# Performance work log

Measured on AMD Instinct MI355X. Metric: run time of the kernel, lower is better.

Reference implementation:

```python
import jax, jax.numpy as jnp
import numpy as np

# Geometry constants (from init_kwargs geo)
VIEWS = 512
NDET = 736
NX = 256
NY = 256
EXTENT = 2
CHANNEL = 1
START_ANGLE = 0.0
END_ANGLE = 2.0 * np.pi
SCALE = (END_ANGLE - START_ANGLE) / (2.0 * VIEWS * EXTENT)
SINO_LEN = VIEWS * NDET            # 376832
IDX_LEN = NX * NY * VIEWS * EXTENT  # 67108864


def setup_inputs() -> dict:
    key = jax.random.key(0)
    k1, k2, k3, k4 = jax.random.split(key, 4)
    x = jax.random.normal(k1, (1, CHANNEL, SINO_LEN), dtype=jnp.float32)
    weight = jax.random.uniform(k2, (IDX_LEN,), dtype=jnp.float32)
    bias = jax.random.normal(k3, (NX * NY,), dtype=jnp.float32)
    indices = jax.random.randint(k4, (IDX_LEN,), 0, SINO_LEN, dtype=jnp.int64)
    return {"x": x, "weight": weight, "bias": bias, "indices": indices}


def reference(x, weight, bias, indices):
    # x: [B, C, views*nDetecU]
    sino = x.reshape(-1, CHANNEL, SINO_LEN)
    # Irregular gather: [B, C, NX*NY*views*extent]
    g = jnp.take(sino, indices, axis=2)
    # Learned per-ray weighting (DotProduct)
    g = g * weight  # broadcast over leading [B, C]
    # Group by voxel, sum over views*extent, scale by angular step
    g = g.reshape(-1, CHANNEL, NX * NY, VIEWS * EXTENT)
    out = jnp.sum(g, axis=3) * jnp.float32(SCALE)
    out = out + bias  # broadcast over [B, C]
    out = out.reshape(-1, CHANNEL, NX, NY)
    out = jnp.flip(out, axis=(2, 3))
    return out
```

## Files before the change

### kernel.cpp

```cpp
#include <hip/hip_runtime.h>
#include <hip/hip_fp16.h>
#include <math.h>
#include <stdint.h>

#define VIEWS 512
#define NDET 736
#define NX 256
#define NY 256
#define EXTENT 2
#define SINO_LEN (VIEWS * NDET)
#define NVOX (NX * NY)
#define PER_VOX (VIEWS * EXTENT)

#define SEGB 65536
#define NPASS 12
#define XWS_BYTES (NPASS * SEGB)
#define XWS_HALVES (XWS_BYTES / 2)

__device__ __constant__ float kScale = (float)(M_PI / 1024.0);

typedef int   v4i __attribute__((ext_vector_type(4)));
typedef float v4f __attribute__((ext_vector_type(4)));

__global__ __launch_bounds__(256) void convert_x_kernel(
    const float* __restrict__ x, ushort* __restrict__ xh)
{
    const int t = blockIdx.x * 256 + threadIdx.x;
    const int e = t * 4;
    ushort4 u;
    if (e < SINO_LEN) {
        const float4 v = *(const float4*)(x + e);
        u.x = __half_as_ushort(__float2half(v.x));
        u.y = __half_as_ushort(__float2half(v.y));
        u.z = __half_as_ushort(__float2half(v.z));
        u.w = __half_as_ushort(__float2half(v.w));
    } else {
        u.x = u.y = u.z = u.w = 0;
    }
    *(ushort4*)(xh + e) = u;
}

__global__ __launch_bounds__(512, 4) void backproj_lds_kernel(
    const ushort* __restrict__ xh,
    const float*  __restrict__ weight,
    const float*  __restrict__ bias,
    const int*    __restrict__ indices,
    float*        __restrict__ out)
{
    extern __shared__ unsigned char xs[];

    const int tid  = threadIdx.x;
    const int lane = tid & 63;
    const int wid  = tid >> 6;
    const int vv   = tid >> 5;
    const int q    = tid & 31;

    const int    vox0  = blockIdx.x * 16;
    const size_t pbase = (size_t)(vox0 + vv) * PER_VOX;

    const v4i* ip = (const v4i*)(indices + pbase);
    const v4f* wp = (const v4f*)(weight + pbase);

    v4i i4[8];
    v4f w4[8];
#pragma unroll
    for (int k = 0; k < 8; ++k) i4[k] = __builtin_nontemporal_load(&ip[q + k * 32]);
#pragma unroll
    for (int k = 0; k < 8; ++k) w4[k] = __builtin_nontemporal_load(&wp[q + k * 32]);
#pragma unroll
    for (int k = 0; k < 8; ++k) {
        i4[k].x <<= 1; i4[k].y <<= 1; i4[k].z <<= 1; i4[k].w <<= 1;
    }

    const unsigned sbase = (unsigned)(wid * 8192 + lane * 16);

    float s = 0.0f;

    for (int p = 0; p < NPASS; ++p) {
        const unsigned loB = (unsigned)p * SEGB;

#pragma unroll
        for (int k = 0; k < 8; ++k) {
            const unsigned off = sbase + (unsigned)(k * 1024);
            __builtin_amdgcn_global_load_lds(
                (const __attribute__((address_space(1))) unsigned int*)
                    ((const unsigned char*)xh + loB + off),
                (__attribute__((address_space(3))) unsigned int*)(xs + off),
                16, 0, 0);
        }
        __syncthreads();

#pragma unroll
        for (int k = 0; k < 8; ++k) {
            {
                const unsigned off = (unsigned)i4[k].x - loB;
                const bool in = off < (unsigned)SEGB;
                const unsigned a = in ? off : 0u;
                const float val = __half2float(*(const __half*)(xs + a));
                s = fmaf(val, in ? w4[k].x : 0.0f, s);
            }
            {
                const unsigned off = (unsigned)i4[k].y - loB;
                const bool in = off < (unsigned)SEGB;
                const unsigned a = in ? off : 0u;
                const float val = __half2float(*(const __half*)(xs + a));
                s = fmaf(val, in ? w4[k].y : 0.0f, s);
            }
            {
                const unsigned off = (unsigned)i4[k].z - loB;
                const bool in = off < (unsigned)SEGB;
                const unsigned a = in ? off : 0u;
                const float val = __half2float(*(const __half*)(xs + a));
                s = fmaf(val, in ? w4[k].z : 0.0f, s);
            }
            {
                const unsigned off = (unsigned)i4[k].w - loB;
                const bool in = off < (unsigned)SEGB;
                const unsigned a = in ? off : 0u;
                const float val = __half2float(*(const __half*)(xs + a));
                s = fmaf(val, in ? w4[k].w : 0.0f, s);
            }
        }
        __syncthreads();
    }

#pragma unroll
    for (int off = 16; off > 0; off >>= 1)
        s += __shfl_xor(s, off, 64);

    if (q == 0) {
        const int v = vox0 + vv;
        out[NVOX - 1 - v] = bias[v] + kScale * s;
    }
}

__global__ __launch_bounds__(256) void backproj_fallback_kernel(
    const float* __restrict__ x,
    const float* __restrict__ weight,
    const float* __restrict__ bias,
    const int*   __restrict__ indices,
    float*       __restrict__ out)
{
    const int wave_in_block = threadIdx.x >> 6;
    const int lane          = threadIdx.x & 63;
    const int v             = blockIdx.x * 4 + wave_in_block;
    const size_t base       = (size_t)v * PER_VOX;

    const v4i* ip = (const v4i*)(indices + base);
    const v4f* wp = (const v4f*)(weight + base);

    v4i i4[4];
#pragma unroll
    for (int k = 0; k < 4; ++k)
        i4[k] = __builtin_nontemporal_load(&ip[lane + k * 64]);

    float g[16];
#pragma unroll
    for (int k = 0; k < 4; ++k) {
        g[4 * k + 0] = x[i4[k].x];
        g[4 * k + 1] = x[i4[k].y];
        g[4 * k + 2] = x[i4[k].z];
        g[4 * k + 3] = x[i4[k].w];
    }

    v4f w4[4];
#pragma unroll
    for (int k = 0; k < 4; ++k)
        w4[k] = __builtin_nontemporal_load(&wp[lane + k * 64]);

    float s = 0.0f;
#pragma unroll
    for (int k = 0; k < 4; ++k) {
        s += g[4 * k + 0] * w4[k].x;
        s += g[4 * k + 1] * w4[k].y;
        s += g[4 * k + 2] * w4[k].z;
        s += g[4 * k + 3] * w4[k].w;
    }

#pragma unroll
    for (int off = 32; off > 0; off >>= 1)
        s += __shfl_down(s, off, 64);

    if (lane == 0)
        out[NVOX - 1 - v] = bias[v] + kScale * s;
}

extern "C" void kernel_launch(void* const* d_in, const int* in_sizes, int n_in,
                              void* d_out, int out_size, void* d_ws, size_t ws_size,
                              hipStream_t stream) {
    const float* x       = (const float*)d_in[0];
    const float* weight  = (const float*)d_in[1];
    const float* bias    = (const float*)d_in[2];
    const int*   indices = (const int*)d_in[3];
    float*       out     = (float*)d_out;

    if (ws_size >= (size_t)XWS_BYTES) {
        ushort* xh = (ushort*)d_ws;
        convert_x_kernel<<<XWS_HALVES / 4 / 256, 256, 0, stream>>>(x, xh);
        backproj_lds_kernel<<<NVOX / 16, 512, SEGB, stream>>>(
            xh, weight, bias, indices, out);
    } else {
        backproj_fallback_kernel<<<NVOX / 4, 256, 0, stream>>>(
            x, weight, bias, indices, out);
    }
}
```

Measured before the change: 613.1 us.

## Use 128KB LDS segments with register-staged prefetch and 1024-thread blocks

Doubles the LDS segment to 128KB so only 6 passes over the fp16 sinogram are needed instead of 12, and grows blocks to 1024 threads covering 32 voxels. The next segment is prefetched into registers while the current one is being gathered from, replacing the direct global-to-LDS loads. Indices are pre-packed with the pass number in high bits so each in-range test is a subtract and compare, and four accumulators are used instead of one. This halves the number of pass barriers and redundant segment loads, but one block fills the 160KB LDS, so occupancy drops to one block per CU and the kernel relies on the dynamic shared memory attribute being accepted.

After: 938.9 us. +53.1%, slower.

```diff
diff --git a/kernel.cpp b/kernel.cpp
--- a/kernel.cpp
+++ b/kernel.cpp
@@ -12,8 +12,8 @@
 #define NVOX (NX * NY)
 #define PER_VOX (VIEWS * EXTENT)
 
-#define SEGB 65536
-#define NPASS 12
+#define SEGB 131072
+#define NPASS 6
 #define XWS_BYTES (NPASS * SEGB)
 #define XWS_HALVES (XWS_BYTES / 2)
 
@@ -40,7 +40,7 @@
     *(ushort4*)(xh + e) = u;
 }
 
-__global__ __launch_bounds__(512, 4) void backproj_lds_kernel(
+__global__ __launch_bounds__(1024, 4) void backproj_lds2_kernel(
     const ushort* __restrict__ xh,
     const float*  __restrict__ weight,
     const float*  __restrict__ bias,
@@ -49,81 +49,100 @@
 {
     extern __shared__ unsigned char xs[];
 
-    const int tid  = threadIdx.x;
-    const int lane = tid & 63;
-    const int wid  = tid >> 6;
-    const int vv   = tid >> 5;
-    const int q    = tid & 31;
-
-    const int    vox0  = blockIdx.x * 16;
+    const int tid = threadIdx.x;
+    const int vv  = tid >> 5;
+    const int q   = tid & 31;
+
+    const int    vox0  = blockIdx.x * 32;
     const size_t pbase = (size_t)(vox0 + vv) * PER_VOX;
 
     const v4i* ip = (const v4i*)(indices + pbase);
     const v4f* wp = (const v4f*)(weight + pbase);
 
-    v4i i4[8];
+    v4i pk[8];
     v4f w4[8];
 #pragma unroll
-    for (int k = 0; k < 8; ++k) i4[k] = __builtin_nontemporal_load(&ip[q + k * 32]);
+    for (int k = 0; k < 8; ++k) pk[k] = __builtin_nontemporal_load(&ip[q + k * 32]);
 #pragma unroll
     for (int k = 0; k < 8; ++k) w4[k] = __builtin_nontemporal_load(&wp[q + k * 32]);
+
 #pragma unroll
     for (int k = 0; k < 8; ++k) {
-        i4[k].x <<= 1; i4[k].y <<= 1; i4[k].z <<= 1; i4[k].w <<= 1;
-    }
-
-    const unsigned sbase = (unsigned)(wid * 8192 + lane * 16);
-
-    float s = 0.0f;
-
+        int b;
+        b = pk[k].x << 1; pk[k].x = ((b >> 17) << 20) | (b & (SEGB - 1));
+        b = pk[k].y << 1; pk[k].y = ((b >> 17) << 20) | (b & (SEGB - 1));
+        b = pk[k].z << 1; pk[k].z = ((b >> 17) << 20) | (b & (SEGB - 1));
+        b = pk[k].w << 1; pk[k].w = ((b >> 17) << 20) | (b & (SEGB - 1));
+    }
+
+    float4 r[8];
+    const unsigned soff = (unsigned)tid * 16;
+
+#define ISSUE(SEG)                                                          \
+    {                                                                       \
+        const unsigned char* gp = (const unsigned char*)xh +                \
+                                  (size_t)(SEG) * SEGB;                     \
+        _Pragma("unroll")                                                   \
+        for (int k = 0; k < 8; ++k)                                         \
+            r[k] = *(const float4*)(gp + (unsigned)(k * 16384) + soff);     \
+    }
+#define COMMIT()                                                            \
+    {                                                                       \
+        _Pragma("unroll")                                                   \
+        for (int k = 0; k < 8; ++k)                                         \
+            *(float4*)(xs + (unsigned)(k * 16384) + soff) = r[k];           \
+    }
+
+    ISSUE(0);
+    COMMIT();
+    ISSUE(1);
+    __syncthreads();
+
+    float a0 = 0.0f, a1 = 0.0f, a2 = 0.0f, a3 = 0.0f;
+
+#pragma unroll
     for (int p = 0; p < NPASS; ++p) {
-        const unsigned loB = (unsigned)p * SEGB;
+        const unsigned pb = (unsigned)p << 20;
 
 #pragma unroll
         for (int k = 0; k < 8; ++k) {
-            const unsigned off = sbase + (unsigned)(k * 1024);
-            __builtin_amdgcn_global_load_lds(
-                (const __attribute__((address_space(1))) unsigned int*)
-                    ((const unsigned char*)xh + loB + off),
-                (__attribute__((address_space(3))) unsigned int*)(xs + off),
-                16, 0, 0);
+            {
+                const unsigned t = (unsigned)pk[k].x - pb;
+                const unsigned a = t & (SEGB - 1);
+                const float   ws = (t < (unsigned)SEGB) ? w4[k].x : 0.0f;
+                a0 = fmaf(__half2float(*(const __half*)(xs + a)), ws, a0);
+            }
+            {
+                const unsigned t = (unsigned)pk[k].y - pb;
+                const unsigned a = t & (SEGB - 1);
+                const float   ws = (t < (unsigned)SEGB) ? w4[k].y : 0.0f;
+                a1 = fmaf(__half2float(*(const __half*)(xs + a)), ws, a1);
+            }
+            {
+                const unsigned t = (unsigned)pk[k].z - pb;
+                const unsigned a = t & (SEGB - 1);
+                const float   ws = (t < (unsigned)SEGB) ? w4[k].z : 0.0f;
+                a2 = fmaf(__half2float(*(const __half*)(xs + a)), ws, a2);
+            }
+            {
+                const unsigned t = (unsigned)pk[k].w - pb;
+                const unsigned a = t & (SEGB - 1);
+                const float   ws = (t < (unsigned)SEGB) ? w4[k].w : 0.0f;
+                a3 = fmaf(__half2float(*(const __half*)(xs + a)), ws, a3);
+            }
         }
-        __syncthreads();
-
-#pragma unroll
-        for (int k = 0; k < 8; ++k) {
-            {
-                const unsigned off = (unsigned)i4[k].x - loB;
-                const bool in = off < (unsigned)SEGB;
-                const unsigned a = in ? off : 0u;
-                const float val = __half2float(*(const __half*)(xs + a));
-                s = fmaf(val, in ? w4[k].x : 0.0f, s);
-            }
-            {
-                const unsigned off = (unsigned)i4[k].y - loB;
-                const bool in = off < (unsigned)SEGB;
-                const unsigned a = in ? off : 0u;
-                const float val = __half2float(*(const __half*)(xs + a));
-                s = fmaf(val, in ? w4[k].y : 0.0f, s);
-            }
-            {
-                const unsigned off = (unsigned)i4[k].z - loB;
-                const bool in = off < (unsigned)SEGB;
-                const unsigned a = in ? off : 0u;
-                const float val = __half2float(*(const __half*)(xs + a));
-                s = fmaf(val, in ? w4[k].z : 0.0f, s);
-            }
-            {
-                const unsigned off = (unsigned)i4[k].w - loB;
-                const bool in = off < (unsigned)SEGB;
-                const unsigned a = in ? off : 0u;
-                const float val = __half2float(*(const __half*)(xs + a));
-                s = fmaf(val, in ? w4[k].w : 0.0f, s);
-            }
+
+        if (p < NPASS - 1) {
+            __syncthreads();
+            COMMIT();
+            if (p < NPASS - 2) ISSUE(p + 2);
+            __syncthreads();
         }
-        __syncthreads();
-    }
-
+    }
+#undef ISSUE
+#undef COMMIT
+
+    float s = a0 + a1 + a2 + a3;
 #pragma unroll
     for (int off = 16; off > 0; off >>= 1)
         s += __shfl_xor(s, off, 64);
@@ -195,9 +214,16 @@
     float*       out     = (float*)d_out;
 
     if (ws_size >= (size_t)XWS_BYTES) {
+        static bool attr_done = false;
+        if (!attr_done) {
+            (void)hipFuncSetAttribute((const void*)backproj_lds2_kernel,
+                                      hipFuncAttributeMaxDynamicSharedMemorySize,
+                                      SEGB);
+            attr_done = true;
+        }
         ushort* xh = (ushort*)d_ws;
         convert_x_kernel<<<XWS_HALVES / 4 / 256, 256, 0, stream>>>(x, xh);
-        backproj_lds_kernel<<<NVOX / 16, 512, SEGB, stream>>>(
+        backproj_lds2_kernel<<<NVOX / 32, 1024, SEGB, stream>>>(
             xh, weight, bias, indices, out);
     } else {
         backproj_fallback_kernel<<<NVOX / 4, 256, 0, stream>>>(
```
